# Kernel optimization log

Measured on AMD Instinct MI355X. Metric: run time of the kernel, lower is better.

Reference implementation:

```python
import jax, jax.numpy as jnp
import numpy as np

SOW_INIT = 1e-10  # sum_of_weights_initial_value
EPS = 1e-8       # torch.nn.CosineSimilarity default eps


def setup_inputs() -> dict:
    key = jax.random.key(0)
    k1, k2, k3 = jax.random.split(key, 3)
    input_image = jax.random.normal(k1, (1, 3, 224, 224), dtype=jnp.float32)
    masks = jax.random.uniform(k2, (1000, 224, 224), dtype=jnp.float32)
    # Linear encoder: flattened image [3*224*224] -> feature dim 128
    W = jax.random.normal(k3, (3, 224, 224, 128), dtype=jnp.float32) * 0.01
    return {"input_image": input_image, "masks": masks, "W": W}


def reference(input_image, masks, W):
    img = input_image[0]  # [3, H, W]
    # Encoder applied to (img * mask): rep_n = sum_chw (img*mask)[c,h,w] * W[c,h,w,f]
    # Precompute A[h,w,f] = sum_c img[c,h,w] * W[c,h,w,f] so masked reps never
    # materialize the [N,3,H,W] masked-image tensor.
    A = jnp.einsum('chw,chwf->hwf', img, W)          # [H, W, F]
    rep0 = jnp.sum(A, axis=(0, 1))                   # unmasked representation [F]
    reps = jnp.einsum('nhw,hwf->nf', masks, A)       # masked representations [N, F]

    # Cosine similarity (dim=1), clamped norms as in torch
    n0 = jnp.maximum(jnp.linalg.norm(rep0), EPS)
    nr = jnp.maximum(jnp.linalg.norm(reps, axis=1), EPS)
    sims = (reps @ rep0) / (nr * n0)                 # [N]

    H, Wd = masks.shape[1], masks.shape[2]
    imp0 = jnp.zeros((H, Wd), dtype=jnp.float32)
    unc0 = jnp.zeros((H, Wd), dtype=jnp.float32)
    sow0 = jnp.full((H, Wd), SOW_INIT, dtype=jnp.float32)

    def step(carry, inp):
        imp, unc, sow = carry
        m, s = inp  # mask [H,W], similarity scalar
        sow = sow + m
        prev = imp
        imp = imp + m * (s - imp) / sow
        unc = unc + (s - imp) * (s - prev) * m
        return (imp, unc, sow), None

    (imp, unc, sow), _ = jax.lax.scan(step, (imp0, unc0, sow0), (masks, sims))
    return jnp.stack([imp, unc, sow])  # [3, H, W]
```

## Files before the change

### kernel.cpp

```cpp
#include <hip/hip_runtime.h>
#include <stdint.h>

#define HWN 50176
#define NM  1000
#define FD  128
#define NSPLIT 49
#define KSTEPS 32
#define NSCAN 8
#define NPB 125

typedef __attribute__((ext_vector_type(8))) short short8;
typedef __attribute__((ext_vector_type(4))) float f32x4;

__device__ __forceinline__ unsigned short f2bf(float x) {
    union { float f; unsigned u; } v; v.f = x;
    unsigned r = v.u + 0x7FFFu + ((v.u >> 16) & 1u);
    return (unsigned short)(r >> 16);
}

#define AS1(p) ((const __attribute__((address_space(1))) unsigned int*)(p))
#define AS3(p) ((__attribute__((address_space(3))) unsigned int*)(p))

__global__ __launch_bounds__(256) void k_encode(const float* __restrict__ img,
                                                const float* __restrict__ Wt,
                                                unsigned short* __restrict__ Bpack,
                                                float* __restrict__ rep0part)
{
    const int t = threadIdx.x;
    const int f = t & 127;
    const int kt = blockIdx.x * 2 + (t >> 7);
    const int hw0 = kt * 32;
    float vals[32];
    float rsum = 0.f;
#pragma unroll
    for (int e = 0; e < 32; ++e) {
        const int hw = hw0 + e;
        float a = img[hw] * Wt[(size_t)hw * FD + f];
        a = fmaf(img[HWN + hw],     Wt[(size_t)(HWN + hw) * FD + f], a);
        a = fmaf(img[2 * HWN + hw], Wt[(size_t)(2 * HWN + hw) * FD + f], a);
        vals[e] = a;
        rsum += a;
    }
    char* tile = (char*)Bpack + (size_t)kt * 8192 + f * 64;
#pragma unroll
    for (int j = 0; j < 4; ++j) {
        short8 pk;
#pragma unroll
        for (int e = 0; e < 8; ++e) pk[e] = (short)f2bf(vals[j * 8 + e]);
        *reinterpret_cast<short8*>(tile + ((j ^ (f & 3)) << 4)) = pk;
    }
    __shared__ float red[256];
    red[t] = rsum;
    __syncthreads();
    if (t < 128) rep0part[(size_t)blockIdx.x * 128 + f] = red[t] + red[t + 128];
}

__global__ __launch_bounds__(256) void k_rep0red(const float* __restrict__ rep0part,
                                                 float* __restrict__ rep0)
{
    const int f = blockIdx.x;
    float s = 0.f;
    for (int b = threadIdx.x; b < 784; b += 256) s += rep0part[(size_t)b * 128 + f];
    __shared__ float red[256];
    red[threadIdx.x] = s;
    __syncthreads();
    for (int o = 128; o > 0; o >>= 1) {
        if (threadIdx.x < o) red[threadIdx.x] += red[threadIdx.x + o];
        __syncthreads();
    }
    if (threadIdx.x == 0) rep0[f] = red[0];
}

__global__ __launch_bounds__(512, 4) void k_gemm(const float* __restrict__ masks,
                                                 const unsigned short* __restrict__ Bpack,
                                                 float* __restrict__ partial)
{
    __shared__ __align__(16) unsigned short Bs[2][4096];

    const int t = threadIdx.x;
    const int wv = t >> 6, lane = t & 63;
    const int lrow = lane & 15, lslot = lane >> 4;
    const int mtile = blockIdx.x, split = blockIdx.y;

    int row = mtile * 128 + wv * 16 + lrow;
    if (row >= NM) row = NM - 1;
    const float* aptr = masks + (size_t)row * HWN + split * 1024 + lslot * 8;
    const char* bsrc = (const char*)Bpack + (size_t)(split * KSTEPS) * 8192 + t * 16;
    char* dst0 = (char*)&Bs[0][0] + t * 16;
    char* dst1 = (char*)&Bs[1][0] + t * 16;
    const int rdoff = lrow * 64 + ((lslot ^ (lrow & 3)) << 4);

    f32x4 acc[8];
#pragma unroll
    for (int i = 0; i < 8; ++i) acc[i] = f32x4{0.f, 0.f, 0.f, 0.f};

    __builtin_amdgcn_global_load_lds(AS1(bsrc), AS3(dst0), 16, 0, 0);
    f32x4 a0 = *reinterpret_cast<const f32x4*>(aptr);
    f32x4 a1 = *reinterpret_cast<const f32x4*>(aptr + 4);

    for (int ks = 0; ks < KSTEPS; ++ks) {
        const int cur = ks & 1;
        __syncthreads();
        if (ks + 1 < KSTEPS)
            __builtin_amdgcn_global_load_lds(AS1(bsrc + (size_t)(ks + 1) * 8192),
                                             AS3(cur ? dst0 : dst1), 16, 0, 0);
        const int kn = (ks + 1 < KSTEPS) ? (ks + 1) : ks;
        f32x4 na0 = *reinterpret_cast<const f32x4*>(aptr + kn * 32);
        f32x4 na1 = *reinterpret_cast<const f32x4*>(aptr + kn * 32 + 4);

        short8 apk;
        apk[0] = (short)f2bf(a0[0]); apk[1] = (short)f2bf(a0[1]);
        apk[2] = (short)f2bf(a0[2]); apk[3] = (short)f2bf(a0[3]);
        apk[4] = (short)f2bf(a1[0]); apk[5] = (short)f2bf(a1[1]);
        apk[6] = (short)f2bf(a1[2]); apk[7] = (short)f2bf(a1[3]);

        const char* bbase = (const char*)&Bs[cur][0] + rdoff;
#pragma unroll
        for (int ft = 0; ft < 8; ++ft) {
            short8 bfv = *reinterpret_cast<const short8*>(bbase + ft * 1024);
            acc[ft] = __builtin_amdgcn_mfma_f32_16x16x32_bf16(apk, bfv, acc[ft], 0, 0, 0);
        }
        a0 = na0; a1 = na1;
    }

    const int crow = mtile * 128 + wv * 16 + (lslot << 2);
    float* pb = partial + ((size_t)split * 1024 + crow) * FD + lrow;
#pragma unroll
    for (int ft = 0; ft < 8; ++ft)
#pragma unroll
        for (int r = 0; r < 4; ++r)
            pb[(size_t)r * FD + ft * 16] = acc[ft][r];
}

__global__ __launch_bounds__(128) void k_sims(const float* __restrict__ partial,
                                              const float* __restrict__ rep0,
                                              float* __restrict__ sims)
{
    const int n = blockIdx.x;
    const int f = threadIdx.x;
    float r = 0.f;
    for (int s = 0; s < NSPLIT; ++s)
        r += partial[((size_t)s * 1024 + n) * FD + f];
    const float r0 = rep0[f];
    __shared__ float red0[128], red1[128], red2[128];
    red0[f] = r * r0;
    red1[f] = r * r;
    red2[f] = r0 * r0;
    __syncthreads();
    for (int o = 64; o > 0; o >>= 1) {
        if (f < o) {
            red0[f] += red0[f + o];
            red1[f] += red1[f + o];
            red2[f] += red2[f + o];
        }
        __syncthreads();
    }
    if (f == 0) {
        const float nr = fmaxf(sqrtf(red1[0]), 1e-8f);
        const float nz = fmaxf(sqrtf(red2[0]), 1e-8f);
        sims[n] = red0[0] / (nr * nz);
    }
}

__global__ __launch_bounds__(256) void k_colsums(const float* __restrict__ masks,
                                                 const float* __restrict__ sims,
                                                 float* __restrict__ Spart)
{
    __shared__ float s1v[NPB], s2v[NPB];
    const int t = threadIdx.x;
    const int split = blockIdx.y;
    if (t < NPB) {
        const float s = sims[split * NPB + t];
        s1v[t] = s;
        s2v[t] = s * s;
    }
    __syncthreads();
    const int pix = blockIdx.x * 256 + t;
    const float* mp = masks + (size_t)split * NPB * HWN + pix;
    float s0 = 0.f, s1 = 0.f, s2 = 0.f;
#pragma unroll 5
    for (int i = 0; i < NPB; ++i) {
        const float m = mp[(size_t)i * HWN];
        s0 += m;
        s1 = fmaf(m, s1v[i], s1);
        s2 = fmaf(m, s2v[i], s2);
    }
    float* sp = Spart + (size_t)split * 3 * HWN + pix;
    sp[0] = s0;
    sp[HWN] = s1;
    sp[2 * HWN] = s2;
}

__global__ __launch_bounds__(256) void k_final(const float* __restrict__ Spart,
                                               float* __restrict__ out)
{
    const int pix = blockIdx.x * 256 + threadIdx.x;
    float s0 = 0.f, s1 = 0.f, s2 = 0.f;
#pragma unroll
    for (int sp = 0; sp < NSCAN; ++sp) {
        const float* p = Spart + (size_t)sp * 3 * HWN + pix;
        s0 += p[0];
        s1 += p[HWN];
        s2 += p[2 * HWN];
    }
    const float sow = 1e-10f + s0;
    const float imp = s1 / sow;
    const float unc = fmaf(-imp, s1, s2);
    out[pix] = imp;
    out[HWN + pix] = unc;
    out[2 * HWN + pix] = sow;
}

extern "C" void kernel_launch(void* const* d_in, const int* in_sizes, int n_in,
                              void* d_out, int out_size, void* d_ws, size_t ws_size,
                              hipStream_t stream) {
    const float* img   = (const float*)d_in[0];
    const float* masks = (const float*)d_in[1];
    const float* Wt    = (const float*)d_in[2];
    float* out = (float*)d_out;

    char* ws = (char*)d_ws;
    unsigned short* Bpack = (unsigned short*)ws;
    float* partial  = (float*)(ws + 12845056);
    float* rep0part = partial;
    float* rep0     = (float*)(ws + 38535168);
    float* sims     = (float*)(ws + 38535680);
    float* Spart    = (float*)ws;

    hipLaunchKernelGGL(k_encode,  dim3(784), dim3(256), 0, stream, img, Wt, Bpack, rep0part);
    hipLaunchKernelGGL(k_rep0red, dim3(128), dim3(256), 0, stream, rep0part, rep0);
    hipLaunchKernelGGL(k_gemm,    dim3(8, NSPLIT), dim3(512), 0, stream, masks, Bpack, partial);
    hipLaunchKernelGGL(k_sims,    dim3(NM), dim3(128), 0, stream, partial, rep0, sims);
    hipLaunchKernelGGL(k_colsums, dim3(196, NSCAN), dim3(256), 0, stream, masks, sims, Spart);
    hipLaunchKernelGGL(k_final,   dim3(196), dim3(256), 0, stream, Spart, out);
}
```

Measured before the change: 126.6 us.

## Shrink GEMM blocks, vectorize colsums/final, add nontemporal stores and bf16 pack intrinsic

The GEMM now uses 256-thread blocks covering 64 mask rows, so the grid doubles and each thread issues two LDS async loads per K-step to fill the B tile. Float-to-bf16 packing switches to the HIP paired conversion intrinsic. Colsums and final are vectorized to float4 per thread, and colsums splits the mask list into 20 chunks instead of 8. Nontemporal loads and stores are added for the partial-sum buffers. Together these aim to raise parallelism and memory-bandwidth efficiency, at the cost of loading B more often and reducing more partial sums.

```diff
diff --git a/kernel.cpp b/kernel.cpp
--- a/kernel.cpp
+++ b/kernel.cpp
@@ -1,4 +1,5 @@
 #include <hip/hip_runtime.h>
+#include <hip/hip_bf16.h>
 #include <stdint.h>
 
 #define HWN 50176
@@ -6,8 +7,8 @@
 #define FD  128
 #define NSPLIT 49
 #define KSTEPS 32
-#define NSCAN 8
-#define NPB 125
+#define NSCAN 20
+#define NPB 50
 
 typedef __attribute__((ext_vector_type(8))) short short8;
 typedef __attribute__((ext_vector_type(4))) float f32x4;
@@ -71,7 +72,7 @@
     if (threadIdx.x == 0) rep0[f] = red[0];
 }
 
-__global__ __launch_bounds__(512, 4) void k_gemm(const float* __restrict__ masks,
+__global__ __launch_bounds__(256, 4) void k_gemm(const float* __restrict__ masks,
                                                  const unsigned short* __restrict__ Bpack,
                                                  float* __restrict__ partial)
 {
@@ -82,7 +83,7 @@
     const int lrow = lane & 15, lslot = lane >> 4;
     const int mtile = blockIdx.x, split = blockIdx.y;
 
-    int row = mtile * 128 + wv * 16 + lrow;
+    int row = mtile * 64 + wv * 16 + lrow;
     if (row >= NM) row = NM - 1;
     const float* aptr = masks + (size_t)row * HWN + split * 1024 + lslot * 8;
     const char* bsrc = (const char*)Bpack + (size_t)(split * KSTEPS) * 8192 + t * 16;
@@ -95,41 +96,45 @@
     for (int i = 0; i < 8; ++i) acc[i] = f32x4{0.f, 0.f, 0.f, 0.f};
 
     __builtin_amdgcn_global_load_lds(AS1(bsrc), AS3(dst0), 16, 0, 0);
+    __builtin_amdgcn_global_load_lds(AS1(bsrc + 4096), AS3(dst0 + 4096), 16, 0, 0);
     f32x4 a0 = *reinterpret_cast<const f32x4*>(aptr);
     f32x4 a1 = *reinterpret_cast<const f32x4*>(aptr + 4);
 
     for (int ks = 0; ks < KSTEPS; ++ks) {
         const int cur = ks & 1;
         __syncthreads();
-        if (ks + 1 < KSTEPS)
-            __builtin_amdgcn_global_load_lds(AS1(bsrc + (size_t)(ks + 1) * 8192),
-                                             AS3(cur ? dst0 : dst1), 16, 0, 0);
+        if (ks + 1 < KSTEPS) {
+            char* nd = cur ? dst0 : dst1;
+            const char* nsrc = bsrc + (size_t)(ks + 1) * 8192;
+            __builtin_amdgcn_global_load_lds(AS1(nsrc), AS3(nd), 16, 0, 0);
+            __builtin_amdgcn_global_load_lds(AS1(nsrc + 4096), AS3(nd + 4096), 16, 0, 0);
+        }
         const int kn = (ks + 1 < KSTEPS) ? (ks + 1) : ks;
         f32x4 na0 = *reinterpret_cast<const f32x4*>(aptr + kn * 32);
         f32x4 na1 = *reinterpret_cast<const f32x4*>(aptr + kn * 32 + 4);
 
-        short8 apk;
-        apk[0] = (short)f2bf(a0[0]); apk[1] = (short)f2bf(a0[1]);
-        apk[2] = (short)f2bf(a0[2]); apk[3] = (short)f2bf(a0[3]);
-        apk[4] = (short)f2bf(a1[0]); apk[5] = (short)f2bf(a1[1]);
-        apk[6] = (short)f2bf(a1[2]); apk[7] = (short)f2bf(a1[3]);
+        union { short8 s; __hip_bfloat162 h[4]; } apk;
+        apk.h[0] = __float22bfloat162_rn(float2{a0[0], a0[1]});
+        apk.h[1] = __float22bfloat162_rn(float2{a0[2], a0[3]});
+        apk.h[2] = __float22bfloat162_rn(float2{a1[0], a1[1]});
+        apk.h[3] = __float22bfloat162_rn(float2{a1[2], a1[3]});
 
         const char* bbase = (const char*)&Bs[cur][0] + rdoff;
 #pragma unroll
         for (int ft = 0; ft < 8; ++ft) {
             short8 bfv = *reinterpret_cast<const short8*>(bbase + ft * 1024);
-            acc[ft] = __builtin_amdgcn_mfma_f32_16x16x32_bf16(apk, bfv, acc[ft], 0, 0, 0);
+            acc[ft] = __builtin_amdgcn_mfma_f32_16x16x32_bf16(apk.s, bfv, acc[ft], 0, 0, 0);
         }
         a0 = na0; a1 = na1;
     }
 
-    const int crow = mtile * 128 + wv * 16 + (lslot << 2);
+    const int crow = mtile * 64 + wv * 16 + (lslot << 2);
     float* pb = partial + ((size_t)split * 1024 + crow) * FD + lrow;
 #pragma unroll
     for (int ft = 0; ft < 8; ++ft)
 #pragma unroll
         for (int r = 0; r < 4; ++r)
-            pb[(size_t)r * FD + ft * 16] = acc[ft][r];
+            __builtin_nontemporal_store(acc[ft][r], pb + (size_t)r * FD + ft * 16);
 }
 
 __global__ __launch_bounds__(128) void k_sims(const float* __restrict__ partial,
@@ -140,7 +145,7 @@
     const int f = threadIdx.x;
     float r = 0.f;
     for (int s = 0; s < NSPLIT; ++s)
-        r += partial[((size_t)s * 1024 + n) * FD + f];
+        r += __builtin_nontemporal_load(partial + ((size_t)s * 1024 + n) * FD + f);
     const float r0 = rep0[f];
     __shared__ float red0[128], red1[128], red2[128];
     red0[f] = r * r0;
@@ -175,40 +180,48 @@
         s2v[t] = s * s;
     }
     __syncthreads();
-    const int pix = blockIdx.x * 256 + t;
+    const int pix = (blockIdx.x * 256 + t) * 4;
     const float* mp = masks + (size_t)split * NPB * HWN + pix;
-    float s0 = 0.f, s1 = 0.f, s2 = 0.f;
+    f32x4 s0 = {0.f,0.f,0.f,0.f}, s1 = s0, s2 = s0;
 #pragma unroll 5
     for (int i = 0; i < NPB; ++i) {
-        const float m = mp[(size_t)i * HWN];
+        const f32x4 m = *reinterpret_cast<const f32x4*>(mp + (size_t)i * HWN);
+        const float a = s1v[i], b = s2v[i];
         s0 += m;
-        s1 = fmaf(m, s1v[i], s1);
-        s2 = fmaf(m, s2v[i], s2);
+#pragma unroll
+        for (int e = 0; e < 4; ++e) {
+            s1[e] = fmaf(m[e], a, s1[e]);
+            s2[e] = fmaf(m[e], b, s2[e]);
+        }
     }
     float* sp = Spart + (size_t)split * 3 * HWN + pix;
-    sp[0] = s0;
-    sp[HWN] = s1;
-    sp[2 * HWN] = s2;
+    __builtin_nontemporal_store(s0, reinterpret_cast<f32x4*>(sp));
+    __builtin_nontemporal_store(s1, reinterpret_cast<f32x4*>(sp + HWN));
+    __builtin_nontemporal_store(s2, reinterpret_cast<f32x4*>(sp + 2 * HWN));
 }
 
 __global__ __launch_bounds__(256) void k_final(const float* __restrict__ Spart,
                                                float* __restrict__ out)
 {
-    const int pix = blockIdx.x * 256 + threadIdx.x;
-    float s0 = 0.f, s1 = 0.f, s2 = 0.f;
-#pragma unroll
+    const int pix = (blockIdx.x * 256 + threadIdx.x) * 4;
+    f32x4 s0 = {0.f,0.f,0.f,0.f}, s1 = s0, s2 = s0;
+#pragma unroll 4
     for (int sp = 0; sp < NSCAN; ++sp) {
         const float* p = Spart + (size_t)sp * 3 * HWN + pix;
-        s0 += p[0];
-        s1 += p[HWN];
-        s2 += p[2 * HWN];
-    }
-    const float sow = 1e-10f + s0;
-    const float imp = s1 / sow;
-    const float unc = fmaf(-imp, s1, s2);
-    out[pix] = imp;
-    out[HWN + pix] = unc;
-    out[2 * HWN + pix] = sow;
+        s0 += __builtin_nontemporal_load(reinterpret_cast<const f32x4*>(p));
+        s1 += __builtin_nontemporal_load(reinterpret_cast<const f32x4*>(p + HWN));
+        s2 += __builtin_nontemporal_load(reinterpret_cast<const f32x4*>(p + 2 * HWN));
+    }
+    f32x4 imp, unc, sow;
+#pragma unroll
+    for (int e = 0; e < 4; ++e) {
+        sow[e] = 1e-10f + s0[e];
+        imp[e] = s1[e] / sow[e];
+        unc[e] = fmaf(-imp[e], s1[e], s2[e]);
+    }
+    *reinterpret_cast<f32x4*>(out + pix) = imp;
+    *reinterpret_cast<f32x4*>(out + HWN + pix) = unc;
+    *reinterpret_cast<f32x4*>(out + 2 * HWN + pix) = sow;
 }
 
 extern "C" void kernel_launch(void* const* d_in, const int* in_sizes, int n_in,
@@ -229,8 +242,8 @@
 
     hipLaunchKernelGGL(k_encode,  dim3(784), dim3(256), 0, stream, img, Wt, Bpack, rep0part);
     hipLaunchKernelGGL(k_rep0red, dim3(128), dim3(256), 0, stream, rep0part, rep0);
-    hipLaunchKernelGGL(k_gemm,    dim3(8, NSPLIT), dim3(512), 0, stream, masks, Bpack, partial);
+    hipLaunchKernelGGL(k_gemm,    dim3(16, NSPLIT), dim3(256), 0, stream, masks, Bpack, partial);
     hipLaunchKernelGGL(k_sims,    dim3(NM), dim3(128), 0, stream, partial, rep0, sims);
-    hipLaunchKernelGGL(k_colsums, dim3(196, NSCAN), dim3(256), 0, stream, masks, sims, Spart);
-    hipLaunchKernelGGL(k_final,   dim3(196), dim3(256), 0, stream, Spart, out);
-}
+    hipLaunchKernelGGL(k_colsums, dim3(49, NSCAN), dim3(256), 0, stream, masks, sims, Spart);
+    hipLaunchKernelGGL(k_final,   dim3(49), dim3(256), 0, stream, Spart, out);
+}
```

Result: slower. 148.5 us (+17.2%).
